# Kernel tuning notes

Hardware: AMD Instinct MI355X
Metric: run time of the kernel (lower is better)

## Reference

```python
import jax, jax.numpy as jnp
import numpy as np

H = 2048
V = 50257
M = 64

def setup_inputs() -> dict:
    key = jax.random.key(0)
    ks = jax.random.split(key, 14)
    s = 0.02  # weight init scale for numerical sanity
    return {
        "input_tok": jax.random.randint(ks[0], (1,), 0, V),
        "hidden": jax.random.normal(ks[1], (1, 1, H), jnp.float32),
        "encoder_outputs": jax.random.normal(ks[2], (M, H), jnp.float32),
        "emb": jax.random.normal(ks[3], (V, H), jnp.float32) * s,
        "attn_w": jax.random.normal(ks[4], (M, 2 * H), jnp.float32) * s,
        "attn_b": jax.random.normal(ks[5], (M,), jnp.float32) * s,
        "comb_w": jax.random.normal(ks[6], (H, 2 * H), jnp.float32) * s,
        "comb_b": jax.random.normal(ks[7], (H,), jnp.float32) * s,
        "w_ih": jax.random.normal(ks[8], (3 * H, H), jnp.float32) * s,
        "w_hh": jax.random.normal(ks[9], (3 * H, H), jnp.float32) * s,
        "b_ih": jax.random.normal(ks[10], (3 * H,), jnp.float32) * s,
        "b_hh": jax.random.normal(ks[11], (3 * H,), jnp.float32) * s,
        "out_w": jax.random.normal(ks[12], (V, H), jnp.float32) * s,
        "out_b": jax.random.normal(ks[13], (V,), jnp.float32) * s,
    }

def reference(input_tok, hidden, encoder_outputs, emb, attn_w, attn_b,
              comb_w, comb_b, w_ih, w_hh, b_ih, b_hh, out_w, out_b):
    # embedded: [1, H] (dropout is eval-mode identity)
    embedded = emb[input_tok].reshape(1, H)
    h0 = hidden[0]  # [1, H]
    # Bahdanau-style attention over encoder outputs
    attn_weights = jax.nn.softmax(
        jnp.concatenate([embedded, h0], axis=1) @ attn_w.T + attn_b, axis=1)  # [1, M]
    attn_applied = attn_weights @ encoder_outputs  # [1, H]
    # combine + relu
    x = jnp.concatenate([embedded, attn_applied], axis=1) @ comb_w.T + comb_b
    x = jax.nn.relu(x)  # [1, H] -> GRU input
    # single GRU cell step, PyTorch gate order (r, z, n)
    gi = x @ w_ih.T + b_ih   # [1, 3H]
    gh = h0 @ w_hh.T + b_hh  # [1, 3H]
    i_r, i_z, i_n = jnp.split(gi, 3, axis=1)
    h_r, h_z, h_n = jnp.split(gh, 3, axis=1)
    r = jax.nn.sigmoid(i_r + h_r)
    z = jax.nn.sigmoid(i_z + h_z)
    n = jnp.tanh(i_n + r * h_n)
    h_new = (1.0 - z) * n + z * h0  # [1, H]
    # output projection + log-softmax over vocab
    log_probs = jax.nn.log_softmax(h_new @ out_w.T + out_b, axis=1)  # [1, V]
    return (log_probs, h_new[None], attn_weights)
```

## Files before the change

kernel.cpp:

```cpp
#include <hip/hip_runtime.h>
#include <math.h>

#define H 2048
#define V 50257
#define M 64
#define NEG_BIG (-1.0e30f)

#define NB5 6283
#define NB6 197

typedef float f4 __attribute__((ext_vector_type(4)));

__device__ inline f4 ntload(const f4* p) { return __builtin_nontemporal_load(p); }
__device__ inline float dot4(f4 a, f4 b) { return a.x*b.x + a.y*b.y + a.z*b.z + a.w*b.w; }

__device__ inline float wred_sum(float v) {
#pragma unroll
    for (int o = 32; o >= 1; o >>= 1) v += __shfl_down(v, o);
    return v;
}

__global__ void k_indep(const int* __restrict__ tok, const float* __restrict__ hidden,
                        const float* __restrict__ emb, const float* __restrict__ attn_w,
                        const float* __restrict__ attn_b, const float* __restrict__ w_hh,
                        const float* __restrict__ b_hh, const float* __restrict__ comb_w,
                        float* __restrict__ scores, float* __restrict__ gh,
                        float* __restrict__ pc) {
    const int t = threadIdx.x, lane = t & 63, wid = t >> 6;
    const int b = blockIdx.x;
    if (b < 64) {
        const int m = b;
        const float* erow = emb + (size_t)tok[0] * H;
        const f4* w4 = (const f4*)(attn_w + (size_t)m * 2 * H);
        float acc = 0.f;
        for (int i = t; i < 1024; i += 256) {
            f4 w = ntload(w4 + i);
            int k = i * 4;
            f4 c = (k < H) ? *(const f4*)(erow + k) : *(const f4*)(hidden + (k - H));
            acc += dot4(w, c);
        }
        __shared__ float sred[4];
        float s = wred_sum(acc);
        if (lane == 0) sred[wid] = s;
        __syncthreads();
        if (t == 0) scores[m] = sred[0] + sred[1] + sred[2] + sred[3] + attn_b[m];
    } else if (b < 832) {
        const int j0 = ((b - 64) * 4 + wid) * 2;
        const f4* w0 = (const f4*)(w_hh + (size_t)j0 * H);
        const f4* w1 = (const f4*)(w_hh + (size_t)(j0 + 1) * H);
        const f4* h4 = (const f4*)hidden;
        float a0 = 0.f, a1 = 0.f;
#pragma unroll
        for (int it = 0; it < 8; ++it) {
            int i = it * 64 + lane;
            f4 hv = h4[i];
            a0 += dot4(ntload(w0 + i), hv);
            a1 += dot4(ntload(w1 + i), hv);
        }
        a0 = wred_sum(a0); a1 = wred_sum(a1);
        if (lane == 0) { gh[j0] = a0 + b_hh[j0]; gh[j0 + 1] = a1 + b_hh[j0 + 1]; }
    } else {
        const int r = (b - 832) * 4 + wid;
        const float* erow = emb + (size_t)tok[0] * H;
        const f4* w4 = (const f4*)(comb_w + (size_t)r * 2 * H);
        const f4* e4 = (const f4*)erow;
        float acc = 0.f;
#pragma unroll
        for (int it = 0; it < 8; ++it) {
            int i = it * 64 + lane;
            acc += dot4(ntload(w4 + i), e4[i]);
        }
        acc = wred_sum(acc);
        if (lane == 0) pc[r] = acc;
    }
}

__global__ void k_sm_aa(const float* __restrict__ scores, const float* __restrict__ enc,
                        float* __restrict__ aw_out, float* __restrict__ attn_applied) {
    __shared__ float w[M];
    int t = threadIdx.x;
    if (t < 64) {
        float s = scores[t];
        float mx = s;
#pragma unroll
        for (int o = 32; o >= 1; o >>= 1) mx = fmaxf(mx, __shfl_xor(mx, o));
        float e = expf(s - mx);
        float sum = e;
#pragma unroll
        for (int o = 32; o >= 1; o >>= 1) sum += __shfl_xor(sum, o);
        float aw = e / sum;
        w[t] = aw;
        if (blockIdx.x == 0) aw_out[t] = aw;
    }
    __syncthreads();
    int h = blockIdx.x * 256 + t;
    float acc = 0.f;
#pragma unroll 8
    for (int m = 0; m < M; ++m) acc += w[m] * enc[(size_t)m * H + h];
    attn_applied[h] = acc;
}

__global__ void k_combine2(const float* __restrict__ comb_w, const float* __restrict__ comb_b,
                           const float* __restrict__ aa, const float* __restrict__ pc,
                           float* __restrict__ x_out) {
    int r = (blockIdx.x * blockDim.x + threadIdx.x) >> 6;
    int lane = threadIdx.x & 63;
    const f4* w4 = (const f4*)(comb_w + (size_t)r * 2 * H + H);
    const f4* a4 = (const f4*)aa;
    float acc = 0.f;
#pragma unroll
    for (int it = 0; it < 8; ++it) {
        int i = it * 64 + lane;
        acc += dot4(ntload(w4 + i), a4[i]);
    }
    acc = wred_sum(acc);
    if (lane == 0) x_out[r] = fmaxf(pc[r] + acc + comb_b[r], 0.f);
}

__global__ void k_gates(const float* __restrict__ hidden, const float* __restrict__ w_ih,
                        const float* __restrict__ b_ih, const float* __restrict__ x,
                        const float* __restrict__ gh, float* __restrict__ h_out) {
    int j = (blockIdx.x * blockDim.x + threadIdx.x) >> 6;
    int lane = threadIdx.x & 63;
    const f4* x4 = (const f4*)x;
    const f4* wr = (const f4*)(w_ih + (size_t)j * H);
    const f4* wz = (const f4*)(w_ih + (size_t)(H + j) * H);
    const f4* wn = (const f4*)(w_ih + (size_t)(2 * H + j) * H);
    float ar = 0.f, az = 0.f, an = 0.f;
#pragma unroll
    for (int it = 0; it < 8; ++it) {
        int i = it * 64 + lane;
        f4 xv = x4[i];
        ar += dot4(ntload(wr + i), xv);
        az += dot4(ntload(wz + i), xv);
        an += dot4(ntload(wn + i), xv);
    }
    ar = wred_sum(ar); az = wred_sum(az); an = wred_sum(an);
    if (lane == 0) {
        float r = 1.f / (1.f + expf(-(ar + b_ih[j] + gh[j])));
        float z = 1.f / (1.f + expf(-(az + b_ih[H + j] + gh[H + j])));
        float n = tanhf(an + b_ih[2 * H + j] + r * gh[2 * H + j]);
        h_out[j] = (1.f - z) * n + z * hidden[j];
    }
}

__global__ void k_logits(const float* __restrict__ out_w, const float* __restrict__ out_b,
                         const float* __restrict__ hnew, float* __restrict__ logits,
                         float2* __restrict__ part) {
    const int t = threadIdx.x, lane = t & 63, wid = t >> 6;
    const int base = (blockIdx.x * 4 + wid) * 2;
    const int row0 = base, row1 = base + 1;
    const bool v0 = row0 < V, v1 = row1 < V;
    const f4* w0 = (const f4*)(out_w + (size_t)(v0 ? row0 : 0) * H);
    const f4* w1 = (const f4*)(out_w + (size_t)(v1 ? row1 : 0) * H);
    const f4* h4 = (const f4*)hnew;
    float a0 = 0.f, a1 = 0.f;
#pragma unroll
    for (int it = 0; it < 8; ++it) {
        int i = it * 64 + lane;
        f4 h = h4[i];
        a0 += dot4(ntload(w0 + i), h);
        a1 += dot4(ntload(w1 + i), h);
    }
    a0 = wred_sum(a0); a1 = wred_sum(a1);
    float m = NEG_BIG, s = 0.f;
    if (lane == 0) {
        if (v0) { float lg = a0 + out_b[row0]; logits[row0] = lg; m = lg; s = 1.f; }
        if (v1) { float lg = a1 + out_b[row1]; logits[row1] = lg;
                  float mm = fmaxf(m, lg); s = s * expf(m - mm) + expf(lg - mm); m = mm; }
    }
    __shared__ float2 lms[4];
    if (lane == 0) lms[wid] = make_float2(m, s);
    __syncthreads();
    if (t == 0) {
        float gm = NEG_BIG, gs = 0.f;
#pragma unroll
        for (int i2 = 0; i2 < 4; ++i2) {
            float m2 = lms[i2].x, s2 = lms[i2].y;
            float mm = fmaxf(gm, m2);
            gs = gs * expf(gm - mm) + s2 * expf(m2 - mm);
            gm = mm;
        }
        part[blockIdx.x] = make_float2(gm, gs);
    }
}

__global__ void k_logsoftmax(float* __restrict__ logits, const float2* __restrict__ part) {
    const int t = threadIdx.x;
    float m = NEG_BIG, s = 0.f;
    for (int i = t; i < NB5; i += 256) {
        float2 p = part[i];
        float mm = fmaxf(m, p.x);
        s = s * expf(m - mm) + p.y * expf(p.x - mm);
        m = mm;
    }
    __shared__ float sm[256], ss[256];
    sm[t] = m; ss[t] = s;
    __syncthreads();
    for (int o = 128; o >= 1; o >>= 1) {
        if (t < o) {
            float m2 = sm[t + o], s2 = ss[t + o];
            float mm = fmaxf(sm[t], m2);
            ss[t] = ss[t] * expf(sm[t] - mm) + s2 * expf(m2 - mm);
            sm[t] = mm;
        }
        __syncthreads();
    }
    float lse = sm[0] + logf(ss[0]);
    int i = blockIdx.x * 256 + t;
    if (i < V) logits[i] -= lse;
}

extern "C" void kernel_launch(void* const* d_in, const int* in_sizes, int n_in,
                              void* d_out, int out_size, void* d_ws, size_t ws_size,
                              hipStream_t stream) {
    const int*   tok     = (const int*)d_in[0];
    const float* hidden  = (const float*)d_in[1];
    const float* enc     = (const float*)d_in[2];
    const float* emb     = (const float*)d_in[3];
    const float* attn_w  = (const float*)d_in[4];
    const float* attn_b  = (const float*)d_in[5];
    const float* comb_w  = (const float*)d_in[6];
    const float* comb_b  = (const float*)d_in[7];
    const float* w_ih    = (const float*)d_in[8];
    const float* w_hh    = (const float*)d_in[9];
    const float* b_ih    = (const float*)d_in[10];
    const float* b_hh    = (const float*)d_in[11];
    const float* out_w   = (const float*)d_in[12];
    const float* out_b   = (const float*)d_in[13];

    float* out = (float*)d_out;
    float* logp  = out;
    float* hout  = out + V;
    float* awout = out + V + H;

    float* ws = (float*)d_ws;
    float*  AA   = ws;
    float*  X    = ws + 2048;
    float*  SC   = ws + 4096;
    float*  GH   = ws + 4160;
    float*  PC   = ws + 10304;
    float2* PART = (float2*)(ws + 12352);

    k_indep     <<<1344, 256, 0, stream>>>(tok, hidden, emb, attn_w, attn_b, w_hh, b_hh,
                                           comb_w, SC, GH, PC);
    k_sm_aa     <<<8,    256, 0, stream>>>(SC, enc, awout, AA);
    k_combine2  <<<512,  256, 0, stream>>>(comb_w, comb_b, AA, PC, X);
    k_gates     <<<512,  256, 0, stream>>>(hidden, w_ih, b_ih, X, GH, hout);
    k_logits    <<<NB5,  256, 0, stream>>>(out_w, out_b, hout, logp, PART);
    k_logsoftmax<<<NB6,  256, 0, stream>>>(logp, PART);
}
```

Baseline: 107.1 us.

## Prefetch output-projection weights during small kernels and widen logits blocks

Extra blocks are added to the attention-softmax and combine kernels. They read the first slices of out_w with ordinary loads, so that part of the large vocab projection matrix is pulled into cache while those latency-bound kernels run. The logits kernel moves to 512-thread blocks covering 16 rows each, which halves the number of partial max/sum entries. The goal is to overlap part of the dominant out_w stream with earlier dependent stages. The risk is that the warm-up traffic competes for bandwidth with the small kernels, and the prefetched lines may be evicted before k_logits reads them.

```diff
diff --git a/kernel.cpp b/kernel.cpp
--- a/kernel.cpp
+++ b/kernel.cpp
@@ -6,8 +6,9 @@
 #define M 64
 #define NEG_BIG (-1.0e30f)
 
-#define NB5 6283
+#define NB5 3142
 #define NB6 197
+#define NWARM 256
 
 typedef float f4 __attribute__((ext_vector_type(4)));
 
@@ -18,6 +19,18 @@
 #pragma unroll
     for (int o = 32; o >= 1; o >>= 1) v += __shfl_down(v, o);
     return v;
+}
+
+__device__ inline void warm_outw(const float* __restrict__ out_w, int q, int t,
+                                 float* __restrict__ dummy) {
+    const f4* w4 = (const f4*)out_w + (size_t)q * 4096;
+    float acc = 0.f;
+#pragma unroll 4
+    for (int i = t; i < 4096; i += 256) {
+        f4 v = w4[i];
+        acc += v.x + v.y + v.z + v.w;
+    }
+    if (acc == -12345.678f) dummy[0] = acc;
 }
 
 __global__ void k_indep(const int* __restrict__ tok, const float* __restrict__ hidden,
@@ -76,9 +89,14 @@
 }
 
 __global__ void k_sm_aa(const float* __restrict__ scores, const float* __restrict__ enc,
-                        float* __restrict__ aw_out, float* __restrict__ attn_applied) {
+                        float* __restrict__ aw_out, float* __restrict__ attn_applied,
+                        const float* __restrict__ out_w, float* __restrict__ dummy) {
+    int t = threadIdx.x;
+    if (blockIdx.x >= 8) {
+        warm_outw(out_w, blockIdx.x - 8, t, dummy);
+        return;
+    }
     __shared__ float w[M];
-    int t = threadIdx.x;
     if (t < 64) {
         float s = scores[t];
         float mx = s;
@@ -102,9 +120,15 @@
 
 __global__ void k_combine2(const float* __restrict__ comb_w, const float* __restrict__ comb_b,
                            const float* __restrict__ aa, const float* __restrict__ pc,
-                           float* __restrict__ x_out) {
-    int r = (blockIdx.x * blockDim.x + threadIdx.x) >> 6;
-    int lane = threadIdx.x & 63;
+                           float* __restrict__ x_out, const float* __restrict__ out_w,
+                           float* __restrict__ dummy) {
+    int t = threadIdx.x;
+    if (blockIdx.x >= 512) {
+        warm_outw(out_w, NWARM + (blockIdx.x - 512), t, dummy);
+        return;
+    }
+    int r = (blockIdx.x * 256 + t) >> 6;
+    int lane = t & 63;
     const f4* w4 = (const f4*)(comb_w + (size_t)r * 2 * H + H);
     const f4* a4 = (const f4*)aa;
     float acc = 0.f;
@@ -144,11 +168,12 @@
     }
 }
 
-__global__ void k_logits(const float* __restrict__ out_w, const float* __restrict__ out_b,
-                         const float* __restrict__ hnew, float* __restrict__ logits,
-                         float2* __restrict__ part) {
+__global__ void __launch_bounds__(512) k_logits(
+        const float* __restrict__ out_w, const float* __restrict__ out_b,
+        const float* __restrict__ hnew, float* __restrict__ logits,
+        float2* __restrict__ part) {
     const int t = threadIdx.x, lane = t & 63, wid = t >> 6;
-    const int base = (blockIdx.x * 4 + wid) * 2;
+    const int base = blockIdx.x * 16 + wid * 2;
     const int row0 = base, row1 = base + 1;
     const bool v0 = row0 < V, v1 = row1 < V;
     const f4* w0 = (const f4*)(out_w + (size_t)(v0 ? row0 : 0) * H);
@@ -169,13 +194,13 @@
         if (v1) { float lg = a1 + out_b[row1]; logits[row1] = lg;
                   float mm = fmaxf(m, lg); s = s * expf(m - mm) + expf(lg - mm); m = mm; }
     }
-    __shared__ float2 lms[4];
+    __shared__ float2 lms[8];
     if (lane == 0) lms[wid] = make_float2(m, s);
     __syncthreads();
     if (t == 0) {
         float gm = NEG_BIG, gs = 0.f;
 #pragma unroll
-        for (int i2 = 0; i2 < 4; ++i2) {
+        for (int i2 = 0; i2 < 8; ++i2) {
             float m2 = lms[i2].x, s2 = lms[i2].y;
             float mm = fmaxf(gm, m2);
             gs = gs * expf(gm - mm) + s2 * expf(m2 - mm);
@@ -240,13 +265,14 @@
     float*  SC   = ws + 4096;
     float*  GH   = ws + 4160;
     float*  PC   = ws + 10304;
-    float2* PART = (float2*)(ws + 12352);
-
-    k_indep     <<<1344, 256, 0, stream>>>(tok, hidden, emb, attn_w, attn_b, w_hh, b_hh,
-                                           comb_w, SC, GH, PC);
-    k_sm_aa     <<<8,    256, 0, stream>>>(SC, enc, awout, AA);
-    k_combine2  <<<512,  256, 0, stream>>>(comb_w, comb_b, AA, PC, X);
-    k_gates     <<<512,  256, 0, stream>>>(hidden, w_ih, b_ih, X, GH, hout);
-    k_logits    <<<NB5,  256, 0, stream>>>(out_w, out_b, hout, logp, PART);
-    k_logsoftmax<<<NB6,  256, 0, stream>>>(logp, PART);
-}
+    float*  DUM  = ws + 12352;
+    float2* PART = (float2*)(ws + 12354);
+
+    k_indep     <<<1344,      256, 0, stream>>>(tok, hidden, emb, attn_w, attn_b, w_hh, b_hh,
+                                                comb_w, SC, GH, PC);
+    k_sm_aa     <<<8 + NWARM, 256, 0, stream>>>(SC, enc, awout, AA, out_w, DUM);
+    k_combine2  <<<512+NWARM, 256, 0, stream>>>(comb_w, comb_b, AA, PC, X, out_w, DUM);
+    k_gates     <<<512,       256, 0, stream>>>(hidden, w_ih, b_ih, X, GH, hout);
+    k_logits    <<<NB5,       512, 0, stream>>>(out_w, out_b, hout, logp, PART);
+    k_logsoftmax<<<NB6,       256, 0, stream>>>(logp, PART);
+}
```

After: 111.2 us. 1.04x slower.
